# Optimization experiments

Hardware: AMD Instinct MI355X
Metric: run time of the kernel (lower is better)

Reference implementation:

```python
import jax, jax.numpy as jnp
import numpy as np
from functools import partial

# ---- constants from params ----
NODES = 64          # cfg_s[0]: nodes per graph
HEADS, BASES = 8, 4 # EGConv num_heads / num_bases (aggregators = ['symnorm'], A=1)
THRESH, LENS = 0.5, 0.5
ENC_THRESH, ENC_LENS = 0.5, 0.5
DECAY = 0.2
LSTM_ALPHA = 2.0

# ---- surrogate spike functions ----
@partial(jax.custom_vjp, nondiff_argnums=(1, 2))
def atan_spike(x, thresh, alpha):
    return (x > thresh).astype(x.dtype)

def _atan_fwd(x, thresh, alpha):
    return atan_spike(x, thresh, alpha), x

def _atan_bwd(thresh, alpha, x, g):
    grad = (alpha / 2.0) / (1.0 + (jnp.pi / 2.0 * alpha * (x - thresh)) ** 2)
    return (g * grad,)

atan_spike.defvjp(_atan_fwd, _atan_bwd)

@partial(jax.custom_vjp, nondiff_argnums=(1,))
def erf_spike(x, alpha):
    return (x > 0).astype(x.dtype)

def _erf_fwd(x, alpha):
    return erf_spike(x, alpha), x

def _erf_bwd(alpha, x, g):
    grad = alpha / (2.0 * jnp.sqrt(jnp.pi)) * jnp.exp(-(alpha * x / 2.0) ** 2)
    return (g * grad,)

erf_spike.defvjp(_erf_fwd, _erf_bwd)


def setup_inputs() -> dict:
    key = jax.random.key(0)
    N, Cin, T = 16384, 8, 32
    Cenc, Cgnn = 128, 128
    Fh = Cgnn // HEADS
    HID, FC1, NC = 512, 256, 4
    E = 262144
    ks = jax.random.split(key, 12)

    def w(k, shape, fan_in):
        return jax.random.normal(k, shape, jnp.float32) / np.float32(np.sqrt(fan_in))

    return {
        "x": jax.random.normal(ks[0], (N, Cin, T), jnp.float32),
        "edge_index": jax.random.randint(ks[1], (2, E), 0, N, dtype=jnp.int32),
        "enc_W": w(ks[2], (Cin, Cenc), Cin),
        "enc_b": jnp.zeros((Cenc,), jnp.float32),
        "bases_W": w(ks[3], (Cenc, BASES * Fh), Cenc),
        "bases_b": jnp.zeros((BASES * Fh,), jnp.float32),
        "comb_W": w(ks[4], (Cenc, HEADS * BASES), Cenc),
        "comb_b": jnp.zeros((HEADS * BASES,), jnp.float32),
        "conv_bias": jnp.zeros((Cgnn,), jnp.float32),
        "W_ih": w(ks[5], (NODES * Cgnn, 4 * HID), NODES * Cgnn),
        "W_hh": w(ks[6], (HID, 4 * HID), HID),
        "b_ih": jnp.zeros((4 * HID,), jnp.float32),
        "b_hh": jnp.zeros((4 * HID,), jnp.float32),
        "fc1_W": w(ks[7], (HID, FC1), HID),
        "fc1_b": jnp.zeros((FC1,), jnp.float32),
        "fc2_W": w(ks[8], (FC1, NC), FC1),
        "fc2_b": jnp.zeros((NC,), jnp.float32),
    }


def reference(x, edge_index, enc_W, enc_b, bases_W, bases_b, comb_W, comb_b,
              conv_bias, W_ih, W_hh, b_ih, b_hh, fc1_W, fc1_b, fc2_W, fc2_b):
    N, Cin, T = x.shape
    S = N // NODES
    Cgnn = conv_bias.shape[0]
    Fh = Cgnn // HEADS
    HID = W_hh.shape[0]
    FC1 = fc1_b.shape[0]
    NC = fc2_b.shape[0]

    # EGConv symnorm graph structure with self-loops (fixed across time)
    loop = jnp.arange(N, dtype=edge_index.dtype)
    s_all = jnp.concatenate([edge_index[0], loop])
    d_all = jnp.concatenate([edge_index[1], loop])
    deg = jax.ops.segment_sum(jnp.ones(s_all.shape[0], x.dtype), d_all, num_segments=N)
    dinv = jnp.where(deg > 0, jax.lax.rsqrt(jnp.maximum(deg, 1e-12)), 0.0)
    ew = dinv[s_all] * dinv[d_all]  # [E+N]

    xs = jnp.moveaxis(x, -1, 0)  # [T, N, Cin]

    def step(carry, xt):
        (enc_mem, enc_spike, c1_mem, c1_spike, lh, lc,
         h1_mem, h1_spike, h2_mem, h2_spike, h2_sum) = carry
        # encoding LIF
        enc_mem = enc_mem * DECAY * (1.0 - enc_spike) + xt @ enc_W + enc_b
        enc_spike = atan_spike(enc_mem, ENC_THRESH, ENC_LENS)
        # EGConv (symnorm aggregator, A=1)
        bases = enc_spike @ bases_W + bases_b                       # [N, B*Fh]
        agg = jax.ops.segment_sum(ew[:, None] * bases[s_all], d_all, num_segments=N)
        comb = (enc_spike @ comb_W + comb_b).reshape(N, HEADS, BASES)
        conv = jnp.einsum('nhb,nbf->nhf', comb, agg.reshape(N, BASES, Fh))
        conv = conv.reshape(S, NODES, Cgnn) + conv_bias
        # conv LIF
        c1_mem = c1_mem * DECAY * (1.0 - c1_spike) + conv
        c1_spike = atan_spike(c1_mem, THRESH, LENS)
        # spiking LSTM cell (erf surrogates on all gates)
        xl = c1_spike.reshape(S, NODES * Cgnn)
        gates = xl @ W_ih + b_ih + lh @ W_hh + b_hh
        i, f, g, o = jnp.split(gates, 4, axis=-1)
        i = erf_spike(i, LSTM_ALPHA)
        f = erf_spike(f, LSTM_ALPHA)
        g = erf_spike(g, LSTM_ALPHA)
        o = erf_spike(o, LSTM_ALPHA)
        lc = f * lc + i * g
        lh = lc * o
        # fc1 LIF
        h1_mem = h1_mem * DECAY * (1.0 - h1_spike) + lh @ fc1_W + fc1_b
        h1_spike = atan_spike(h1_mem, THRESH, LENS)
        # fc2 LIF
        h2_mem = h2_mem * DECAY * (1.0 - h2_spike) + h1_spike @ fc2_W + fc2_b
        h2_spike = atan_spike(h2_mem, THRESH, LENS)
        return (enc_mem, enc_spike, c1_mem, c1_spike, lh, lc,
                h1_mem, h1_spike, h2_mem, h2_spike, h2_sum + h2_spike), None

    Cenc = enc_b.shape[0]
    z = lambda shape: jnp.zeros(shape, x.dtype)
    carry0 = (z((N, Cenc)), z((N, Cenc)), z((S, NODES, Cgnn)), z((S, NODES, Cgnn)),
              z((S, HID)), z((S, HID)), z((S, FC1)), z((S, FC1)),
              z((S, NC)), z((S, NC)), z((S, NC)))
    carry, _ = jax.lax.scan(step, carry0, xs)
    h2_sum = carry[-1]
    return h2_sum / jnp.asarray(T, x.dtype)
```

## Files before the change

kernel.cpp:

```cpp
#include <hip/hip_runtime.h>

#define NN      16384
#define TSTEPS  32
#define SG      256
#define NE      262144

#define OFF_ENC_MEM   0u
#define OFF_ENC_SPK   2097152u
#define OFF_C1_MEM    4194304u
#define OFF_C1_SPK    6291456u
#define OFF_LH        8388608u
#define OFF_LC        8519680u
#define OFF_H1_MEM    8650752u
#define OFF_H1_SPK    8716288u
#define OFF_H2_MEM    8781824u
#define OFF_H2_SPK    8782848u
#define OFF_H2_SUM    8783872u
#define ZERO_FLOATS   8784896u
#define OFF_BASES     8784896u
#define OFF_COMB      9833472u
#define OFF_GATES     10357760u
#define OFF_DINV      23464960u
#define OFF_COLW      23481344u
#define FLOAT_END     23743488u
#define IOFF_DEG      0
#define IOFF_FILL     16384
#define IOFF_ROWPTR   32768
#define IOFF_EID      49153
#define IOFF_COL      311297
#define INT_COUNT     573441

__global__ void k_deg(const int* __restrict__ ei, int* __restrict__ deg) {
  int e = blockIdx.x * 256 + threadIdx.x;
  if (e < NE) atomicAdd(&deg[ei[NE + e]], 1);
}

__global__ void k_dinv(const int* __restrict__ deg, float* __restrict__ dinv) {
  int n = blockIdx.x * 256 + threadIdx.x;
  if (n < NN) dinv[n] = __fdiv_rn(1.0f, __fsqrt_rn((float)(deg[n] + 1)));
}

__global__ void k_scan(const int* __restrict__ deg, int* __restrict__ rowp) {
  __shared__ int sdata[1024];
  int tid = threadIdx.x;
  int base = tid * 16;
  int loc[16];
  int sum = 0;
  #pragma unroll
  for (int i = 0; i < 16; ++i) { loc[i] = sum; sum += deg[base + i]; }
  sdata[tid] = sum;
  __syncthreads();
  for (int off = 1; off < 1024; off <<= 1) {
    int v = 0;
    if (tid >= off) v = sdata[tid - off];
    __syncthreads();
    sdata[tid] += v;
    __syncthreads();
  }
  int excl = (tid == 0) ? 0 : sdata[tid - 1];
  #pragma unroll
  for (int i = 0; i < 16; ++i) rowp[base + i] = excl + loc[i];
  if (tid == 1023) rowp[NN] = sdata[1023];
}

__global__ void k_scatter(const int* __restrict__ ei, const int* __restrict__ rowp,
                          int* __restrict__ fill, int* __restrict__ eid) {
  int e = blockIdx.x * 256 + threadIdx.x;
  if (e >= NE) return;
  int d = ei[NE + e];
  int pos = rowp[d] + atomicAdd(&fill[d], 1);
  eid[pos] = e;
}

__global__ void k_sortadj(const int* __restrict__ rowp, int* __restrict__ eid,
                          const int* __restrict__ ei, const float* __restrict__ dinv,
                          int* __restrict__ col, float* __restrict__ colw) {
  int d = blockIdx.x * 256 + threadIdx.x;
  if (d >= NN) return;
  int r0 = rowp[d], r1 = rowp[d + 1];
  for (int i = r0 + 1; i < r1; ++i) {
    int key = eid[i];
    int j = i - 1;
    while (j >= r0 && eid[j] > key) { eid[j + 1] = eid[j]; --j; }
    eid[j + 1] = key;
  }
  for (int i = r0; i < r1; ++i) {
    int s = ei[eid[i]];
    col[i] = s;
    colw[i] = dinv[s];
  }
}

__global__ __launch_bounds__(512) void k_bases_comb(
    const float* __restrict__ x, const float* __restrict__ encW, const float* __restrict__ encB,
    float* __restrict__ enc_mem, float* __restrict__ enc_spk,
    const float* __restrict__ basesW, const float* __restrict__ basesB,
    const float* __restrict__ combW, const float* __restrict__ combB,
    float* __restrict__ bases, float* __restrict__ comb, int t) {
  __shared__ float xs[64][8];
  __shared__ float sp[64 * 129];
  __shared__ float ob[64 * 65];
  __shared__ float oc[64 * 33];
  const int tid = threadIdx.x;
  const int nb = blockIdx.x * 64;
  {
    int n = tid >> 3, c = tid & 7;
    xs[n][c] = x[(size_t)(nb + n) * 256 + (size_t)c * 32 + t];
  }
  __syncthreads();
  #pragma unroll 4
  for (int k = 0; k < 16; ++k) {
    int idx = k * 512 + tid;
    int n = idx >> 7, j = idx & 127;
    int gidx = nb * 128 + idx;
    float dot = 0.f;
    #pragma unroll
    for (int c = 0; c < 8; ++c) dot = __fmaf_rn(xs[n][c], encW[c * 128 + j], dot);
    float m = enc_mem[gidx], s = enc_spk[gidx];
    float nm = __fadd_rn(__fadd_rn(__fmul_rn(__fmul_rn(m, 0.2f), __fsub_rn(1.f, s)), dot), encB[j]);
    enc_mem[gidx] = nm;
    float spk = nm > 0.5f ? 1.f : 0.f;
    enc_spk[gidx] = spk;
    sp[n * 129 + j] = spk;
  }
  __syncthreads();
  const int lane = tid & 63;
  const int w = tid >> 6;
  const float* spn = sp + lane * 129;
  if (w < 4) {
    const int ch0 = w * 16;
    const float* Wp = basesW + ch0;
    float acc[16];
    #pragma unroll
    for (int c = 0; c < 16; ++c) acc[c] = 0.f;
    for (int j = 0; j < 128; ++j) {
      const float s = spn[j];
      const float* wr = Wp + j * 64;
      #pragma unroll
      for (int c = 0; c < 16; ++c) acc[c] = __fmaf_rn(s, wr[c], acc[c]);
    }
    #pragma unroll
    for (int c = 0; c < 16; ++c) ob[lane * 65 + ch0 + c] = acc[c];
  } else {
    const int ch0 = (w - 4) * 8;
    const float* Wp = combW + ch0;
    float acc[8];
    #pragma unroll
    for (int c = 0; c < 8; ++c) acc[c] = 0.f;
    for (int j = 0; j < 128; ++j) {
      const float s = spn[j];
      const float* wr = Wp + j * 32;
      #pragma unroll
      for (int c = 0; c < 8; ++c) acc[c] = __fmaf_rn(s, wr[c], acc[c]);
    }
    #pragma unroll
    for (int c = 0; c < 8; ++c) oc[lane * 33 + ch0 + c] = acc[c];
  }
  __syncthreads();
  #pragma unroll
  for (int r = 0; r < 8; ++r) {
    int idx = r * 512 + tid;
    int n = idx >> 6, ch = idx & 63;
    bases[(size_t)(nb + n) * 64 + ch] = __fadd_rn(ob[n * 65 + ch], basesB[ch]);
  }
  #pragma unroll
  for (int r = 0; r < 4; ++r) {
    int idx = r * 512 + tid;
    int n = idx >> 5, ch = idx & 31;
    comb[(size_t)(nb + n) * 32 + ch] = __fadd_rn(oc[n * 33 + ch], combB[ch]);
  }
}

__global__ __launch_bounds__(256) void k_aggconv(
    const float* __restrict__ bases, const float* __restrict__ comb,
    const float* __restrict__ dinv, const int* __restrict__ rowp,
    const int* __restrict__ col, const float* __restrict__ colw,
    const float* __restrict__ convB,
    float* __restrict__ c1_mem, float* __restrict__ c1_spk) {
  __shared__ float aggl[4][64];
  __shared__ float combl[4][32];
  int w = threadIdx.x >> 6;
  int m = threadIdx.x & 63;
  int d = blockIdx.x * 4 + w;
  float dd = dinv[d];
  int r0 = rowp[d], r1 = rowp[d + 1];
  float acc = 0.f;
  int r = r0;
  for (; r + 4 <= r1; r += 4) {
    const int s0 = col[r], s1 = col[r + 1], s2 = col[r + 2], s3 = col[r + 3];
    const float w0 = colw[r], w1 = colw[r + 1], w2 = colw[r + 2], w3 = colw[r + 3];
    const float b0 = bases[(size_t)s0 * 64 + m];
    const float b1 = bases[(size_t)s1 * 64 + m];
    const float b2 = bases[(size_t)s2 * 64 + m];
    const float b3 = bases[(size_t)s3 * 64 + m];
    acc = __fadd_rn(acc, __fmul_rn(__fmul_rn(w0, dd), b0));
    acc = __fadd_rn(acc, __fmul_rn(__fmul_rn(w1, dd), b1));
    acc = __fadd_rn(acc, __fmul_rn(__fmul_rn(w2, dd), b2));
    acc = __fadd_rn(acc, __fmul_rn(__fmul_rn(w3, dd), b3));
  }
  for (; r < r1; ++r) {
    int s = col[r];
    float ew  = __fmul_rn(colw[r], dd);
    float upd = __fmul_rn(ew, bases[(size_t)s * 64 + m]);
    acc = __fadd_rn(acc, upd);
  }
  {
    float ew  = __fmul_rn(dd, dd);
    float upd = __fmul_rn(ew, bases[(size_t)d * 64 + m]);
    acc = __fadd_rn(acc, upd);
  }
  aggl[w][m] = acc;
  if (m < 32) combl[w][m] = comb[(size_t)d * 32 + m];
  __syncthreads();
  #pragma unroll
  for (int half = 0; half < 2; ++half) {
    int j = m + half * 64;
    int h = j >> 4, f = j & 15;
    float cv = 0.f;
    #pragma unroll
    for (int b = 0; b < 4; ++b)
      cv = __fadd_rn(cv, __fmul_rn(combl[w][h * 4 + b], aggl[w][b * 16 + f]));
    cv = __fadd_rn(cv, convB[j]);
    int idx = d * 128 + j;
    float cm = c1_mem[idx], cs = c1_spk[idx];
    float nm = __fadd_rn(__fmul_rn(__fmul_rn(cm, 0.2f), __fsub_rn(1.f, cs)), cv);
    c1_mem[idx] = nm;
    c1_spk[idx] = nm > 0.5f ? 1.f : 0.f;
  }
}

__global__ __launch_bounds__(512) void k_gates(
    const float* __restrict__ xl, const float* __restrict__ lh,
    const float* __restrict__ Wih, const float* __restrict__ Whh,
    const float* __restrict__ bih, const float* __restrict__ bhh,
    float* __restrict__ gates) {
  __shared__ unsigned short nzk[8192];
  __shared__ float lhs[512];
  __shared__ int wsum[9];
  const int tid = threadIdx.x;
  const int s = blockIdx.x;
  const int lane = tid & 63, wv = tid >> 6;
  const float* __restrict__ srow = xl + (size_t)s * 8192;

  const int kb = tid * 16;
  int cnt = 0;
  #pragma unroll
  for (int i = 0; i < 16; ++i) cnt += (srow[kb + i] != 0.f) ? 1 : 0;
  int pfx = cnt;
  #pragma unroll
  for (int off = 1; off < 64; off <<= 1) {
    int tval = __shfl_up(pfx, off);
    if (lane >= off) pfx += tval;
  }
  if (lane == 63) wsum[wv] = pfx;
  __syncthreads();
  if (tid == 0) {
    int a = 0;
    #pragma unroll
    for (int w = 0; w < 8; ++w) { int tv = wsum[w]; wsum[w] = a; a += tv; }
    wsum[8] = a;
  }
  __syncthreads();
  const int off0 = wsum[wv] + (pfx - cnt);
  {
    int c2 = 0;
    #pragma unroll
    for (int i = 0; i < 16; ++i) {
      if (srow[kb + i] != 0.f) { nzk[off0 + c2] = (unsigned short)(kb + i); ++c2; }
    }
  }
  lhs[tid] = lh[s * 512 + tid];
  __syncthreads();
  const int nnz = wsum[8];

  const int cl = tid * 4;
  const float* __restrict__ Wc = Wih + cl;
  float4 tih = make_float4(0.f, 0.f, 0.f, 0.f);
  float4 pz  = make_float4(0.f, 0.f, 0.f, 0.f);
  int zcur = 0, pend = 384;

#define FOLD(KK)                                                              \
  while ((KK) >= pend) {                                                      \
    tih.x = __fadd_rn(tih.x, pz.x); tih.y = __fadd_rn(tih.y, pz.y);           \
    tih.z = __fadd_rn(tih.z, pz.z); tih.w = __fadd_rn(tih.w, pz.w);           \
    pz.x = 0.f; pz.y = 0.f; pz.z = 0.f; pz.w = 0.f;                           \
    ++zcur; pend = (zcur < 21) ? (pend + 384) : 8192;                         \
  }

  int k0_=0,k1_=0,k2_=0,k3_=0,k4_=0,k5_=0,k6_=0,k7_=0;
  float4 w0_,w1_,w2_,w3_,w4_,w5_,w6_,w7_;
#define PRELOAD(J, KS, WS)                                                    \
  if ((J) < nnz) { KS = nzk[(J)]; WS = *(const float4*)(Wc + (size_t)KS * 2048); }
  PRELOAD(0, k0_, w0_) PRELOAD(1, k1_, w1_) PRELOAD(2, k2_, w2_) PRELOAD(3, k3_, w3_)
  PRELOAD(4, k4_, w4_) PRELOAD(5, k5_, w5_) PRELOAD(6, k6_, w6_) PRELOAD(7, k7_, w7_)

#define STEP(KS, WS, BI, SO) {                                                \
    const int kcur = KS; const float4 wv4 = WS;                               \
    const int nidx = (BI) + (SO) + 8;                                         \
    if (nidx < nnz) { KS = nzk[nidx]; WS = *(const float4*)(Wc + (size_t)KS * 2048); } \
    FOLD(kcur);                                                               \
    pz.x = __fadd_rn(pz.x, wv4.x); pz.y = __fadd_rn(pz.y, wv4.y);             \
    pz.z = __fadd_rn(pz.z, wv4.z); pz.w = __fadd_rn(pz.w, wv4.w);             \
  }

  const int nmain = nnz & ~7;
  for (int i = 0; i < nmain; i += 8) {
    STEP(k0_, w0_, i, 0) STEP(k1_, w1_, i, 1) STEP(k2_, w2_, i, 2) STEP(k3_, w3_, i, 3)
    STEP(k4_, w4_, i, 4) STEP(k5_, w5_, i, 5) STEP(k6_, w6_, i, 6) STEP(k7_, w7_, i, 7)
  }
  for (int i = nmain; i < nnz; ++i) {
    const int kcur = nzk[i];
    const float4 wv4 = *(const float4*)(Wc + (size_t)kcur * 2048);
    FOLD(kcur);
    pz.x = __fadd_rn(pz.x, wv4.x); pz.y = __fadd_rn(pz.y, wv4.y);
    pz.z = __fadd_rn(pz.z, wv4.z); pz.w = __fadd_rn(pz.w, wv4.w);
  }
  for (; zcur < 22; ++zcur) {
    tih.x = __fadd_rn(tih.x, pz.x); tih.y = __fadd_rn(tih.y, pz.y);
    tih.z = __fadd_rn(tih.z, pz.z); tih.w = __fadd_rn(tih.w, pz.w);
    pz.x = 0.f; pz.y = 0.f; pz.z = 0.f; pz.w = 0.f;
  }
#undef STEP
#undef PRELOAD
#undef FOLD

  float4 p22 = make_float4(0.f, 0.f, 0.f, 0.f);
  #pragma unroll 4
  for (int k = 0; k < 384; ++k) {
    const float sv = lhs[k];
    const float4 wv4 = *(const float4*)(Whh + (size_t)k * 2048 + cl);
    p22.x = __fmaf_rn(sv, wv4.x, p22.x); p22.y = __fmaf_rn(sv, wv4.y, p22.y);
    p22.z = __fmaf_rn(sv, wv4.z, p22.z); p22.w = __fmaf_rn(sv, wv4.w, p22.w);
  }
  float4 p23 = make_float4(0.f, 0.f, 0.f, 0.f);
  #pragma unroll 4
  for (int k = 384; k < 512; ++k) {
    const float sv = lhs[k];
    const float4 wv4 = *(const float4*)(Whh + (size_t)k * 2048 + cl);
    p23.x = __fmaf_rn(sv, wv4.x, p23.x); p23.y = __fmaf_rn(sv, wv4.y, p23.y);
    p23.z = __fmaf_rn(sv, wv4.z, p23.z); p23.w = __fmaf_rn(sv, wv4.w, p23.w);
  }
  const float4 bi = *(const float4*)(bih + cl);
  const float4 bh = *(const float4*)(bhh + cl);
  float4 g;
  g.x = __fadd_rn(__fadd_rn(__fadd_rn(tih.x, bi.x), __fadd_rn(p22.x, p23.x)), bh.x);
  g.y = __fadd_rn(__fadd_rn(__fadd_rn(tih.y, bi.y), __fadd_rn(p22.y, p23.y)), bh.y);
  g.z = __fadd_rn(__fadd_rn(__fadd_rn(tih.z, bi.z), __fadd_rn(p22.z, p23.z)), bh.z);
  g.w = __fadd_rn(__fadd_rn(__fadd_rn(tih.w, bi.w), __fadd_rn(p22.w, p23.w)), bh.w);
  *(float4*)(gates + (size_t)s * 2048 + cl) = g;
}

__global__ __launch_bounds__(512) void k_cell(
    const float* __restrict__ gates,
    float* __restrict__ lc, float* __restrict__ lh,
    const float* __restrict__ fc1W, const float* __restrict__ fc1b,
    const float* __restrict__ fc2W, const float* __restrict__ fc2b,
    float* __restrict__ h1_mem, float* __restrict__ h1_spk,
    float* __restrict__ h2_mem, float* __restrict__ h2_spk, float* __restrict__ h2_sum) {
  __shared__ float lhl[512];
  __shared__ float a1buf[256];
  __shared__ float sp1l[256];
  const int s = blockIdx.x;
  const int tid = threadIdx.x;
  {
    const int h = tid;
    const float giv = gates[(size_t)s * 2048 + h];
    const float gfv = gates[(size_t)s * 2048 + 512 + h];
    const float ggv = gates[(size_t)s * 2048 + 1024 + h];
    const float gov = gates[(size_t)s * 2048 + 1536 + h];
    const float iv = giv > 0.f ? 1.f : 0.f;
    const float fv = gfv > 0.f ? 1.f : 0.f;
    const float gv = ggv > 0.f ? 1.f : 0.f;
    const float ov = gov > 0.f ? 1.f : 0.f;
    const int li = s * 512 + h;
    const float lcv = __fadd_rn(__fmul_rn(fv, lc[li]), __fmul_rn(iv, gv));
    lc[li] = lcv;
    const float lhv = __fmul_rn(lcv, ov);
    lh[li] = lhv;
    lhl[h] = lhv;
  }
  __syncthreads();
  float a0 = 0.f;
  if (tid < 256) {
    const int p = tid;
    #pragma unroll 8
    for (int q = 0; q < 384; ++q) a0 = __fmaf_rn(lhl[q], fc1W[q * 256 + p], a0);
  } else {
    const int p = tid - 256;
    float a1 = 0.f;
    #pragma unroll 8
    for (int q = 384; q < 512; ++q) a1 = __fmaf_rn(lhl[q], fc1W[q * 256 + p], a1);
    a1buf[p] = a1;
  }
  __syncthreads();
  if (tid < 256) {
    const int p = tid;
    const float dot1 = __fadd_rn(a0, a1buf[p]);
    const int i1 = s * 256 + p;
    const float m1 = h1_mem[i1], s1o = h1_spk[i1];
    const float nm1 = __fadd_rn(__fadd_rn(__fmul_rn(__fmul_rn(m1, 0.2f), __fsub_rn(1.f, s1o)), dot1), fc1b[p]);
    h1_mem[i1] = nm1;
    const float sp1 = nm1 > 0.5f ? 1.f : 0.f;
    h1_spk[i1] = sp1;
    sp1l[p] = sp1;
  }
  __syncthreads();
  if (tid < 4) {
    const int p = tid;
    float acc = 0.f;
    for (int q = 0; q < 256; ++q) acc = __fmaf_rn(sp1l[q], fc2W[q * 4 + p], acc);
    const int i2 = s * 4 + p;
    const float m2 = h2_mem[i2], s2o = h2_spk[i2];
    const float nm2 = __fadd_rn(__fadd_rn(__fmul_rn(__fmul_rn(m2, 0.2f), __fsub_rn(1.f, s2o)), acc), fc2b[p]);
    h2_mem[i2] = nm2;
    const float sp2 = nm2 > 0.5f ? 1.f : 0.f;
    h2_spk[i2] = sp2;
    h2_sum[i2] = __fadd_rn(h2_sum[i2], sp2);
  }
}

__global__ void k_out(const float* __restrict__ h2_sum, float* __restrict__ out) {
  int i = blockIdx.x * 256 + threadIdx.x;
  if (i < SG * 4) out[i] = __fmul_rn(h2_sum[i], 0.03125f);
}

extern "C" void kernel_launch(void* const* d_in, const int* in_sizes, int n_in,
                              void* d_out, int out_size, void* d_ws, size_t ws_size,
                              hipStream_t stream) {
  const float* x      = (const float*)d_in[0];
  const int*   ei     = (const int*)  d_in[1];
  const float* encW   = (const float*)d_in[2];
  const float* encB   = (const float*)d_in[3];
  const float* basesW = (const float*)d_in[4];
  const float* basesB = (const float*)d_in[5];
  const float* combW  = (const float*)d_in[6];
  const float* combB  = (const float*)d_in[7];
  const float* convB  = (const float*)d_in[8];
  const float* Wih    = (const float*)d_in[9];
  const float* Whh    = (const float*)d_in[10];
  const float* bih    = (const float*)d_in[11];
  const float* bhh    = (const float*)d_in[12];
  const float* fc1W   = (const float*)d_in[13];
  const float* fc1b   = (const float*)d_in[14];
  const float* fc2W   = (const float*)d_in[15];
  const float* fc2b   = (const float*)d_in[16];

  float* ws = (float*)d_ws;
  float* enc_mem = ws + OFF_ENC_MEM;
  float* enc_spk = ws + OFF_ENC_SPK;
  float* c1_mem  = ws + OFF_C1_MEM;
  float* c1_spk  = ws + OFF_C1_SPK;
  float* lhp     = ws + OFF_LH;
  float* lcp     = ws + OFF_LC;
  float* h1_mem  = ws + OFF_H1_MEM;
  float* h1_spk  = ws + OFF_H1_SPK;
  float* h2_mem  = ws + OFF_H2_MEM;
  float* h2_spk  = ws + OFF_H2_SPK;
  float* h2_sum  = ws + OFF_H2_SUM;
  float* bases   = ws + OFF_BASES;
  float* comb    = ws + OFF_COMB;
  float* gates   = ws + OFF_GATES;
  float* dinv    = ws + OFF_DINV;
  float* colw    = ws + OFF_COLW;
  int* ibase = (int*)((char*)d_ws + (size_t)FLOAT_END * 4);
  int* deg  = ibase + IOFF_DEG;
  int* fill = ibase + IOFF_FILL;
  int* rowp = ibase + IOFF_ROWPTR;
  int* eid  = ibase + IOFF_EID;
  int* col  = ibase + IOFF_COL;

  hipMemsetAsync(ws, 0, (size_t)ZERO_FLOATS * 4, stream);
  hipMemsetAsync(ibase, 0, 32768 * 4, stream);

  k_deg    <<<NE / 256, 256, 0, stream>>>(ei, deg);
  k_dinv   <<<NN / 256, 256, 0, stream>>>(deg, dinv);
  k_scan   <<<1, 1024, 0, stream>>>(deg, rowp);
  k_scatter<<<NE / 256, 256, 0, stream>>>(ei, rowp, fill, eid);
  k_sortadj<<<NN / 256, 256, 0, stream>>>(rowp, eid, ei, dinv, col, colw);

  for (int t = 0; t < TSTEPS; ++t) {
    k_bases_comb<<<NN / 64, 512, 0, stream>>>(x, encW, encB, enc_mem, enc_spk,
                                              basesW, basesB, combW, combB, bases, comb, t);
    k_aggconv   <<<NN / 4, 256, 0, stream>>>(bases, comb, dinv, rowp, col, colw, convB, c1_mem, c1_spk);
    k_gates     <<<SG, 512, 0, stream>>>(c1_spk, lhp, Wih, Whh, bih, bhh, gates);
    k_cell      <<<SG, 512, 0, stream>>>(gates, lcp, lhp, fc1W, fc1b, fc2W, fc2b,
                                         h1_mem, h1_spk, h2_mem, h2_spk, h2_sum);
  }
  k_out<<<4, 256, 0, stream>>>(h2_sum, (float*)d_out);
}
```

Before: 6.091 ms.

## Split gates kernel across four column blocks with one output per thread

The LSTM gates kernel now launches a 4×256 grid, and each block handles a quarter of the 2048 gate columns. Each thread computes one column with scalar loads instead of four columns with float4 loads. This gives four times as many blocks for latency hiding on the scattered sparse W_ih row reads. In exchange, each block repeats the nonzero compaction of the spike row and the lh staging, and loads become 4-byte instead of 16-byte per thread.

```diff
diff --git a/kernel.cpp b/kernel.cpp
--- a/kernel.cpp
+++ b/kernel.cpp
@@ -238,7 +238,8 @@
   __shared__ float lhs[512];
   __shared__ int wsum[9];
   const int tid = threadIdx.x;
-  const int s = blockIdx.x;
+  const int s = blockIdx.y;
+  const int q = blockIdx.x;
   const int lane = tid & 63, wv = tid >> 6;
   const float* __restrict__ srow = xl + (size_t)s * 8192;
 
@@ -273,34 +274,31 @@
   __syncthreads();
   const int nnz = wsum[8];
 
-  const int cl = tid * 4;
+  const int cl = q * 512 + tid;
   const float* __restrict__ Wc = Wih + cl;
-  float4 tih = make_float4(0.f, 0.f, 0.f, 0.f);
-  float4 pz  = make_float4(0.f, 0.f, 0.f, 0.f);
+  float tih = 0.f;
+  float pz  = 0.f;
   int zcur = 0, pend = 384;
 
 #define FOLD(KK)                                                              \
   while ((KK) >= pend) {                                                      \
-    tih.x = __fadd_rn(tih.x, pz.x); tih.y = __fadd_rn(tih.y, pz.y);           \
-    tih.z = __fadd_rn(tih.z, pz.z); tih.w = __fadd_rn(tih.w, pz.w);           \
-    pz.x = 0.f; pz.y = 0.f; pz.z = 0.f; pz.w = 0.f;                           \
+    tih = __fadd_rn(tih, pz); pz = 0.f;                                       \
     ++zcur; pend = (zcur < 21) ? (pend + 384) : 8192;                         \
   }
 
   int k0_=0,k1_=0,k2_=0,k3_=0,k4_=0,k5_=0,k6_=0,k7_=0;
-  float4 w0_,w1_,w2_,w3_,w4_,w5_,w6_,w7_;
+  float w0_=0.f,w1_=0.f,w2_=0.f,w3_=0.f,w4_=0.f,w5_=0.f,w6_=0.f,w7_=0.f;
 #define PRELOAD(J, KS, WS)                                                    \
-  if ((J) < nnz) { KS = nzk[(J)]; WS = *(const float4*)(Wc + (size_t)KS * 2048); }
+  if ((J) < nnz) { KS = nzk[(J)]; WS = Wc[(size_t)KS * 2048]; }
   PRELOAD(0, k0_, w0_) PRELOAD(1, k1_, w1_) PRELOAD(2, k2_, w2_) PRELOAD(3, k3_, w3_)
   PRELOAD(4, k4_, w4_) PRELOAD(5, k5_, w5_) PRELOAD(6, k6_, w6_) PRELOAD(7, k7_, w7_)
 
 #define STEP(KS, WS, BI, SO) {                                                \
-    const int kcur = KS; const float4 wv4 = WS;                               \
+    const int kcur = KS; const float wval = WS;                               \
     const int nidx = (BI) + (SO) + 8;                                         \
-    if (nidx < nnz) { KS = nzk[nidx]; WS = *(const float4*)(Wc + (size_t)KS * 2048); } \
+    if (nidx < nnz) { KS = nzk[nidx]; WS = Wc[(size_t)KS * 2048]; }           \
     FOLD(kcur);                                                               \
-    pz.x = __fadd_rn(pz.x, wv4.x); pz.y = __fadd_rn(pz.y, wv4.y);             \
-    pz.z = __fadd_rn(pz.z, wv4.z); pz.w = __fadd_rn(pz.w, wv4.w);             \
+    pz = __fadd_rn(pz, wval);                                                 \
   }
 
   const int nmain = nnz & ~7;
@@ -310,44 +308,26 @@
   }
   for (int i = nmain; i < nnz; ++i) {
     const int kcur = nzk[i];
-    const float4 wv4 = *(const float4*)(Wc + (size_t)kcur * 2048);
+    const float wval = Wc[(size_t)kcur * 2048];
     FOLD(kcur);
-    pz.x = __fadd_rn(pz.x, wv4.x); pz.y = __fadd_rn(pz.y, wv4.y);
-    pz.z = __fadd_rn(pz.z, wv4.z); pz.w = __fadd_rn(pz.w, wv4.w);
-  }
-  for (; zcur < 22; ++zcur) {
-    tih.x = __fadd_rn(tih.x, pz.x); tih.y = __fadd_rn(tih.y, pz.y);
-    tih.z = __fadd_rn(tih.z, pz.z); tih.w = __fadd_rn(tih.w, pz.w);
-    pz.x = 0.f; pz.y = 0.f; pz.z = 0.f; pz.w = 0.f;
-  }
+    pz = __fadd_rn(pz, wval);
+  }
+  for (; zcur < 22; ++zcur) { tih = __fadd_rn(tih, pz); pz = 0.f; }
 #undef STEP
 #undef PRELOAD
 #undef FOLD
 
-  float4 p22 = make_float4(0.f, 0.f, 0.f, 0.f);
+  float p22 = 0.f;
   #pragma unroll 4
-  for (int k = 0; k < 384; ++k) {
-    const float sv = lhs[k];
-    const float4 wv4 = *(const float4*)(Whh + (size_t)k * 2048 + cl);
-    p22.x = __fmaf_rn(sv, wv4.x, p22.x); p22.y = __fmaf_rn(sv, wv4.y, p22.y);
-    p22.z = __fmaf_rn(sv, wv4.z, p22.z); p22.w = __fmaf_rn(sv, wv4.w, p22.w);
-  }
-  float4 p23 = make_float4(0.f, 0.f, 0.f, 0.f);
+  for (int k = 0; k < 384; ++k)
+    p22 = __fmaf_rn(lhs[k], Whh[(size_t)k * 2048 + cl], p22);
+  float p23 = 0.f;
   #pragma unroll 4
-  for (int k = 384; k < 512; ++k) {
-    const float sv = lhs[k];
-    const float4 wv4 = *(const float4*)(Whh + (size_t)k * 2048 + cl);
-    p23.x = __fmaf_rn(sv, wv4.x, p23.x); p23.y = __fmaf_rn(sv, wv4.y, p23.y);
-    p23.z = __fmaf_rn(sv, wv4.z, p23.z); p23.w = __fmaf_rn(sv, wv4.w, p23.w);
-  }
-  const float4 bi = *(const float4*)(bih + cl);
-  const float4 bh = *(const float4*)(bhh + cl);
-  float4 g;
-  g.x = __fadd_rn(__fadd_rn(__fadd_rn(tih.x, bi.x), __fadd_rn(p22.x, p23.x)), bh.x);
-  g.y = __fadd_rn(__fadd_rn(__fadd_rn(tih.y, bi.y), __fadd_rn(p22.y, p23.y)), bh.y);
-  g.z = __fadd_rn(__fadd_rn(__fadd_rn(tih.z, bi.z), __fadd_rn(p22.z, p23.z)), bh.z);
-  g.w = __fadd_rn(__fadd_rn(__fadd_rn(tih.w, bi.w), __fadd_rn(p22.w, p23.w)), bh.w);
-  *(float4*)(gates + (size_t)s * 2048 + cl) = g;
+  for (int k = 384; k < 512; ++k)
+    p23 = __fmaf_rn(lhs[k], Whh[(size_t)k * 2048 + cl], p23);
+
+  const float g = __fadd_rn(__fadd_rn(__fadd_rn(tih, bih[cl]), __fadd_rn(p22, p23)), bhh[cl]);
+  gates[(size_t)s * 2048 + cl] = g;
 }
 
 __global__ __launch_bounds__(512) void k_cell(
@@ -482,7 +462,7 @@
     k_bases_comb<<<NN / 64, 512, 0, stream>>>(x, encW, encB, enc_mem, enc_spk,
                                               basesW, basesB, combW, combB, bases, comb, t);
     k_aggconv   <<<NN / 4, 256, 0, stream>>>(bases, comb, dinv, rowp, col, colw, convB, c1_mem, c1_spk);
-    k_gates     <<<SG, 512, 0, stream>>>(c1_spk, lhp, Wih, Whh, bih, bhh, gates);
+    k_gates     <<<dim3(4, SG), 512, 0, stream>>>(c1_spk, lhp, Wih, Whh, bih, bhh, gates);
     k_cell      <<<SG, 512, 0, stream>>>(gates, lcp, lhp, fc1W, fc1b, fc2W, fc2b,
                                          h1_mem, h1_spk, h2_mem, h2_spk, h2_sum);
   }
```

After: 6.514 ms. +6.9%, slower.
